# Performance work log

Measured on AMD Instinct MI355X. Metric: run time of the kernel, lower is better.

The kernel has to match this reference:

```python
import jax, jax.numpy as jnp
import numpy as np

N_HEADS = 2


def _ln(x, g, b, eps=1e-5):
    m = x.mean(-1, keepdims=True)
    v = ((x - m) ** 2).mean(-1, keepdims=True)
    return (x - m) * jax.lax.rsqrt(v + eps) * g + b


def _mha(x, in_w, in_b, out_w, out_b):
    # standard multi-head self-attention (relative/rotary branch is inert: query_pos=None)
    B, S, d = x.shape
    hd = d // N_HEADS
    qkv = x @ in_w.T + in_b
    q, k, v = jnp.split(qkv, 3, axis=-1)
    q = q.reshape(B, S, N_HEADS, hd)
    k = k.reshape(B, S, N_HEADS, hd)
    v = v.reshape(B, S, N_HEADS, hd)
    scores = jnp.einsum('bqhd,bkhd->bhqk', q, k) / jnp.sqrt(jnp.asarray(hd, x.dtype))
    attn = jax.nn.softmax(scores, axis=-1)
    o = jnp.einsum('bhqk,bkhd->bqhd', attn, v).reshape(B, S, d)
    return o @ out_w.T + out_b


def _forward(x, w1, b1, attn_in_w, attn_in_b, attn_out_w, attn_out_b, ln1_g, ln1_b,
             ffw_w1, ffw_b1, ffw_w2, ffw_b2, ln2_g, ln2_b,
             in_proj_w, conv_w, conv_b, x_proj_w, dt_proj_w, dt_proj_b, A_log, D, out_proj_w,
             w2a, b2a, w2b, b2b, w3a, b3a, w3b, b3b):
    # mlp1: (B,S,1) -> (B,S,d)
    h = x @ w1.T + b1
    # FFWRelativeSelfAttentionModule: 2 layers of post-norm MHA + FFW, take last output
    for i in range(2):
        a = _mha(h, attn_in_w[i], attn_in_b[i], attn_out_w[i], attn_out_b[i])
        h = _ln(h + a, ln1_g[i], ln1_b[i])
        f = jax.nn.relu(h @ ffw_w1[i].T + ffw_b1[i]) @ ffw_w2[i].T + ffw_b2[i]
        h = _ln(h + f, ln2_g[i], ln2_b[i])
    # Mamba block
    xz = h @ in_proj_w.T                       # (B,S,2*di)
    xm, z = jnp.split(xz, 2, axis=-1)          # (B,S,di) each
    S_len = xm.shape[1]
    dcv = conv_w.shape[1]
    xp = jnp.pad(xm, ((0, 0), (dcv - 1, 0), (0, 0)))   # causal depthwise conv1d
    xc = conv_b + sum(conv_w[:, k] * xp[:, k:k + S_len, :] for k in range(dcv))
    xc = jax.nn.silu(xc)
    xdb = xc @ x_proj_w.T                      # (B,S,dt_rank+2*N)
    dt_r = dt_proj_w.shape[1]
    N = A_log.shape[1]
    dti = xdb[..., :dt_r]
    Bm = xdb[..., dt_r:dt_r + N]
    Cm = xdb[..., dt_r + N:]
    dt = jax.nn.softplus(dti @ dt_proj_w.T + dt_proj_b)   # (B,S,di)
    A = -jnp.exp(A_log)                                    # (di,N)

    def step(hst, inp):
        dt_t, B_t, C_t, x_t = inp              # (B,di),(B,N),(B,N),(B,di)
        hst = hst * jnp.exp(dt_t[..., None] * A) + dt_t[..., None] * B_t[:, None, :] * x_t[..., None]
        y = jnp.einsum('bdn,bn->bd', hst, C_t)
        return hst, y

    h0 = jnp.zeros((xc.shape[0], A.shape[0], N), xc.dtype)
    xs = (jnp.swapaxes(dt, 0, 1), jnp.swapaxes(Bm, 0, 1),
          jnp.swapaxes(Cm, 0, 1), jnp.swapaxes(xc, 0, 1))
    _, ys = jax.lax.scan(step, h0, xs)
    y = jnp.swapaxes(ys, 0, 1) + D * xc
    y = y * jax.nn.silu(z)
    h = y @ out_proj_w.T                       # (B,S,d)
    # mlp2 (two stacked Linears, no activation) -> (B,S,1)
    o = (h @ w2a.T + b2a) @ w2b.T + b2b
    o = o.reshape(o.shape[0], -1)              # (B,9)
    # mlp3
    o = jax.nn.relu(o @ w3a.T + b3a) @ w3b.T + b3b
    return o


def setup_inputs() -> dict:
    key = jax.random.key(0)
    ks = jax.random.split(key, 16)
    d, N, dcv, di, dtr, B, S = 256, 16, 4, 512, 16, 4096, 9
    rn = lambda k, shp, s=0.02: jax.random.normal(k, shp, jnp.float32) * s
    return {
        'x': jax.random.normal(ks[0], (B, S, 1), jnp.float32),
        'w1': rn(ks[1], (d, 1), 0.5), 'b1': jnp.zeros((d,)),
        'attn_in_w': rn(ks[2], (2, 3 * d, d)), 'attn_in_b': jnp.zeros((2, 3 * d)),
        'attn_out_w': rn(ks[3], (2, d, d)), 'attn_out_b': jnp.zeros((2, d)),
        'ln1_g': jnp.ones((2, d)), 'ln1_b': jnp.zeros((2, d)),
        'ffw_w1': rn(ks[4], (2, d, d)), 'ffw_b1': jnp.zeros((2, d)),
        'ffw_w2': rn(ks[5], (2, d, d)), 'ffw_b2': jnp.zeros((2, d)),
        'ln2_g': jnp.ones((2, d)), 'ln2_b': jnp.zeros((2, d)),
        'in_proj_w': rn(ks[6], (2 * di, d)),
        'conv_w': rn(ks[7], (di, dcv), 0.2), 'conv_b': jnp.zeros((di,)),
        'x_proj_w': rn(ks[8], (dtr + 2 * N, di)),
        'dt_proj_w': rn(ks[9], (di, dtr), 0.1), 'dt_proj_b': jnp.full((di,), -4.0),
        'A_log': jnp.log(jnp.broadcast_to(jnp.arange(1, N + 1, dtype=jnp.float32), (di, N))),
        'D': jnp.ones((di,)),
        'out_proj_w': rn(ks[10], (d, di)),
        'w2a': rn(ks[11], (32, d)), 'b2a': jnp.zeros((32,)),
        'w2b': rn(ks[12], (1, 32)), 'b2b': jnp.zeros((1,)),
        'w3a': rn(ks[13], (9, 9), 0.3), 'b3a': jnp.zeros((9,)),
        'w3b': rn(ks[14], (1, 9), 0.3), 'b3b': jnp.zeros((1,)),
    }


def reference(x, w1, b1, attn_in_w, attn_in_b, attn_out_w, attn_out_b, ln1_g, ln1_b,
              ffw_w1, ffw_b1, ffw_w2, ffw_b2, ln2_g, ln2_b,
              in_proj_w, conv_w, conv_b, x_proj_w, dt_proj_w, dt_proj_b, A_log, D, out_proj_w,
              w2a, b2a, w2b, b2b, w3a, b3a, w3b, b3b):
    return _forward(x, w1, b1, attn_in_w, attn_in_b, attn_out_w, attn_out_b, ln1_g, ln1_b,
                    ffw_w1, ffw_b1, ffw_w2, ffw_b2, ln2_g, ln2_b,
                    in_proj_w, conv_w, conv_b, x_proj_w, dt_proj_w, dt_proj_b, A_log, D, out_proj_w,
                    w2a, b2a, w2b, b2b, w3a, b3a, w3b, b3b)
```

## Files before the change

kernel.cpp:

```cpp
#include <hip/hip_runtime.h>
#include <hip/hip_bf16.h>
#include <math.h>


#define BATCH 4096

typedef __attribute__((ext_vector_type(8))) short short8;
typedef __attribute__((ext_vector_type(4))) float f32x4;
typedef __attribute__((ext_vector_type(4))) unsigned short u16x4;
typedef unsigned short ushort;

__device__ __forceinline__ ushort f2bf(float f) {
    unsigned u = __float_as_uint(f);
    u += 0x7fffu + ((u >> 16) & 1u);
    return (ushort)(u >> 16);
}

__global__ __launch_bounds__(256) void convw_kernel(
    const float* __restrict__ s0, const float* __restrict__ s1,
    const float* __restrict__ s2, const float* __restrict__ s3,
    const float* __restrict__ s4, const float* __restrict__ s5,
    ushort* __restrict__ dst)
{
    int i = blockIdx.x * 256 + threadIdx.x;
    float v;
    if      (i < 393216)  v = s0[i];
    else if (i < 524288)  v = s1[i - 393216];
    else if (i < 655360)  v = s2[i - 524288];
    else if (i < 786432)  v = s3[i - 655360];
    else if (i < 1048576) v = s4[i - 786432];
    else                  v = s5[i - 1048576];
    dst[i] = f2bf(v);
}

__global__ __launch_bounds__(256) void embed_kernel(
    const float* __restrict__ x, const float* __restrict__ w1,
    const float* __restrict__ b1, float* __restrict__ h,
    ushort* __restrict__ hbf, int r0, int nr)
{
    int i = blockIdx.x * 256 + threadIdx.x;
    if (i >= nr * 256) return;
    int c  = i & 255;
    int row = i >> 8;
    float v = x[r0 + row] * w1[c] + b1[c];
    h[i] = v;
    hbf[i] = f2bf(v);
}

__global__ __launch_bounds__(256) void mgemm_kernel(
    const ushort* __restrict__ A, const ushort* __restrict__ W,
    const float* __restrict__ bias, float* __restrict__ Cf,
    ushort* __restrict__ Cb, const float* __restrict__ yin,
    int M, int N, int K, int lda, int act, int outmode)
{
    __shared__ ushort As[128 * 64];
    __shared__ ushort Bs[128 * 64];

    const int tid  = threadIdx.x;
    const int m0   = blockIdx.x * 128;
    const int n0   = blockIdx.y * 128;
    const int wid  = tid >> 6, lane = tid & 63;
    const int wr   = wid >> 1, wc = wid & 1;
    const int lrow = lane & 15, lk8 = lane >> 4, l7 = lane & 7;
    const int trow = tid >> 3, tchk = tid & 7;

    f32x4 acc[4][4];
    #pragma unroll
    for (int i = 0; i < 4; ++i)
        #pragma unroll
        for (int j = 0; j < 4; ++j)
            acc[i][j] = f32x4{0.f, 0.f, 0.f, 0.f};

    for (int k0 = 0; k0 < K; k0 += 64) {
        #pragma unroll
        for (int p = 0; p < 4; ++p) {
            const int r = p * 32 + trow;
            const short8 av = *reinterpret_cast<const short8*>(
                &A[(size_t)(m0 + r) * lda + k0 + tchk * 8]);
            const short8 wv = *reinterpret_cast<const short8*>(
                &W[(size_t)(n0 + r) * K + k0 + tchk * 8]);
            const int off = r * 64 + ((tchk ^ (r & 7)) << 3);
            *reinterpret_cast<short8*>(&As[off]) = av;
            *reinterpret_cast<short8*>(&Bs[off]) = wv;
        }
        __syncthreads();

        #pragma unroll
        for (int kh = 0; kh < 2; ++kh) {
            short8 af[4], bf[4];
            #pragma unroll
            for (int i = 0; i < 4; ++i) {
                const int ra = wr * 64 + i * 16 + lrow;
                const int rb = wc * 64 + i * 16 + lrow;
                const int sl = ((kh << 2) | lk8) ^ l7;
                af[i] = *reinterpret_cast<const short8*>(&As[ra * 64 + sl * 8]);
                bf[i] = *reinterpret_cast<const short8*>(&Bs[rb * 64 + sl * 8]);
            }
            #pragma unroll
            for (int i = 0; i < 4; ++i)
                #pragma unroll
                for (int j = 0; j < 4; ++j)
                    acc[i][j] = __builtin_amdgcn_mfma_f32_16x16x32_bf16(
                        af[i], bf[j], acc[i][j], 0, 0, 0);
        }
        __syncthreads();
    }

    const int cb = n0 + wc * 64 + lrow;
    const int rb = m0 + wr * 64 + lk8 * 4;
    float bj[4];
    #pragma unroll
    for (int j = 0; j < 4; ++j) bj[j] = bias ? bias[cb + j * 16] : 0.f;

    #pragma unroll
    for (int i = 0; i < 4; ++i) {
        #pragma unroll
        for (int r = 0; r < 4; ++r) {
            const size_t mrow = (size_t)(rb + i * 16 + r) * N;
            #pragma unroll
            for (int j = 0; j < 4; ++j) {
                float v = acc[i][j][r] + bj[j];
                const size_t idx = mrow + cb + j * 16;
                if (act == 1) v = fmaxf(v, 0.f);
                if (outmode == 0) {
                    Cf[idx] = v;
                } else if (outmode == 1) {
                    Cb[idx] = f2bf(v);
                } else {
                    const float sig = 1.f / (1.f + __expf(-v));
                    Cb[idx] = f2bf(yin[idx] * (v * sig));
                }
            }
        }
    }
}

__global__ __launch_bounds__(256) void sgemm_kernel(
    const float* __restrict__ A, const float* __restrict__ W,
    const float* __restrict__ bias, float* __restrict__ C,
    int M, int N, int K, int lda, int act)
{
    __shared__ float As[16][68];
    __shared__ float Ws[16][68];
    const int tid = threadIdx.x;
    const int m0 = blockIdx.y * 64;
    const int n0 = blockIdx.x * 64;
    const int tm = tid >> 4;
    const int tn = tid & 15;
    const int lrow = tid >> 2;
    const int lk   = (tid & 3) * 4;

    float acc[4][4] = {};

    for (int k0 = 0; k0 < K; k0 += 16) {
        {
            int m = m0 + lrow;
            float4 v = make_float4(0.f, 0.f, 0.f, 0.f);
            if (m < M) v = *reinterpret_cast<const float4*>(&A[(size_t)m * lda + k0 + lk]);
            As[lk + 0][lrow] = v.x; As[lk + 1][lrow] = v.y;
            As[lk + 2][lrow] = v.z; As[lk + 3][lrow] = v.w;
            int n = n0 + lrow;
            float4 w = make_float4(0.f, 0.f, 0.f, 0.f);
            if (n < N) w = *reinterpret_cast<const float4*>(&W[(size_t)n * K + k0 + lk]);
            Ws[lk + 0][lrow] = w.x; Ws[lk + 1][lrow] = w.y;
            Ws[lk + 2][lrow] = w.z; Ws[lk + 3][lrow] = w.w;
        }
        __syncthreads();
        #pragma unroll
        for (int k = 0; k < 16; ++k) {
            float4 av = *reinterpret_cast<const float4*>(&As[k][tm * 4]);
            float4 wv = *reinterpret_cast<const float4*>(&Ws[k][tn * 4]);
            float a[4] = {av.x, av.y, av.z, av.w};
            float w[4] = {wv.x, wv.y, wv.z, wv.w};
            #pragma unroll
            for (int i = 0; i < 4; ++i)
                #pragma unroll
                for (int j = 0; j < 4; ++j)
                    acc[i][j] = fmaf(a[i], w[j], acc[i][j]);
        }
        __syncthreads();
    }

    #pragma unroll
    for (int i = 0; i < 4; ++i) {
        int m = m0 + tm * 4 + i;
        if (m >= M) continue;
        #pragma unroll
        for (int j = 0; j < 4; ++j) {
            int n = n0 + tn * 4 + j;
            if (n >= N) continue;
            float v = acc[i][j];
            if (bias) v += bias[n];
            if (act == 1) v = fmaxf(v, 0.f);
            C[(size_t)m * N + n] = v;
        }
    }
}

__global__ __launch_bounds__(128) void attn_kernel(
    const float* __restrict__ qkv, ushort* __restrict__ o, int nb)
{
    __shared__ float q[9][132], kk[9][132], v[9][132];
    __shared__ float sc[9][12];
    const int blk = blockIdx.x;
    if (blk >= nb * 2) return;
    const int b = blk >> 1, head = blk & 1;
    const int t = threadIdx.x;
    const size_t base = (size_t)b * 9 * 768 + (size_t)head * 128;
    #pragma unroll
    for (int s = 0; s < 9; ++s) {
        q[s][t]  = qkv[base + s * 768 + t];
        kk[s][t] = qkv[base + s * 768 + 256 + t];
        v[s][t]  = qkv[base + s * 768 + 512 + t];
    }
    __syncthreads();
    if (t < 81) {
        int qi = t / 9, ki = t % 9;
        float acc = 0.f;
        #pragma unroll 8
        for (int c = 0; c < 128; ++c) acc = fmaf(q[qi][c], kk[ki][c], acc);
        sc[qi][ki] = acc * 0.08838834764831845f;
    }
    __syncthreads();
    if (t < 9) {
        float mx = -1e30f;
        #pragma unroll
        for (int k2 = 0; k2 < 9; ++k2) mx = fmaxf(mx, sc[t][k2]);
        float e[9], sum = 0.f;
        #pragma unroll
        for (int k2 = 0; k2 < 9; ++k2) { e[k2] = __expf(sc[t][k2] - mx); sum += e[k2]; }
        float inv = 1.f / sum;
        #pragma unroll
        for (int k2 = 0; k2 < 9; ++k2) sc[t][k2] = e[k2] * inv;
    }
    __syncthreads();
    #pragma unroll
    for (int qi = 0; qi < 9; ++qi) {
        float acc = 0.f;
        #pragma unroll
        for (int k2 = 0; k2 < 9; ++k2) acc = fmaf(sc[qi][k2], v[k2][t], acc);
        o[(size_t)(b * 9 + qi) * 256 + head * 128 + t] = f2bf(acc);
    }
}

__global__ __launch_bounds__(256) void ln_add_kernel(
    const float* __restrict__ h, const float* __restrict__ a,
    const float* __restrict__ g, const float* __restrict__ bb,
    float* __restrict__ out, ushort* __restrict__ outbf, int nrows)
{
    const int wave = threadIdx.x >> 6;
    const int lane = threadIdx.x & 63;
    const int row = blockIdx.x * 4 + wave;
    if (row >= nrows) return;
    const float4 hv = reinterpret_cast<const float4*>(h + (size_t)row * 256)[lane];
    const float4 av = reinterpret_cast<const float4*>(a + (size_t)row * 256)[lane];
    float x0 = hv.x + av.x, x1 = hv.y + av.y, x2 = hv.z + av.z, x3 = hv.w + av.w;
    float s  = x0 + x1 + x2 + x3;
    float sq = x0 * x0 + x1 * x1 + x2 * x2 + x3 * x3;
    #pragma unroll
    for (int off = 32; off; off >>= 1) {
        s  += __shfl_down(s, off);
        sq += __shfl_down(sq, off);
    }
    s = __shfl(s, 0); sq = __shfl(sq, 0);
    const float mean = s * (1.f / 256.f);
    const float var  = sq * (1.f / 256.f) - mean * mean;
    const float inv  = rsqrtf(var + 1e-5f);
    const float4 gv = reinterpret_cast<const float4*>(g)[lane];
    const float4 bv = reinterpret_cast<const float4*>(bb)[lane];
    float4 ov;
    ov.x = (x0 - mean) * inv * gv.x + bv.x;
    ov.y = (x1 - mean) * inv * gv.y + bv.y;
    ov.z = (x2 - mean) * inv * gv.z + bv.z;
    ov.w = (x3 - mean) * inv * gv.w + bv.w;
    reinterpret_cast<float4*>(out + (size_t)row * 256)[lane] = ov;
    u16x4 bf;
    bf.x = f2bf(ov.x); bf.y = f2bf(ov.y); bf.z = f2bf(ov.z); bf.w = f2bf(ov.w);
    reinterpret_cast<u16x4*>(outbf + (size_t)row * 256)[lane] = bf;
}

__global__ __launch_bounds__(256) void conv_silu_kernel(
    const float* __restrict__ xm, const float* __restrict__ cw,
    const float* __restrict__ cb, float* __restrict__ xc, int nr)
{
    int i = blockIdx.x * 256 + threadIdx.x;
    if (i >= nr * 512) return;
    int c = i & 511;
    int bs = i >> 9;
    int s = bs % 9, b = bs / 9;
    float acc = cb[c];
    #pragma unroll
    for (int k = 0; k < 4; ++k) {
        int sp = s + k - 3;
        if (sp >= 0) acc = fmaf(cw[c * 4 + k], xm[(size_t)(b * 9 + sp) * 512 + c], acc);
    }
    float sig = 1.f / (1.f + __expf(-acc));
    xc[(size_t)bs * 512 + c] = acc * sig;
}

__global__ __launch_bounds__(512) void scan_kernel(
    float* __restrict__ xcy, const float* __restrict__ xdb,
    const float* __restrict__ dt_w, const float* __restrict__ dt_b,
    const float* __restrict__ A_log, const float* __restrict__ Dp)
{
    __shared__ float sx[9 * 48];
    const int c = threadIdx.x;
    const int b = blockIdx.x;
    if (c < 108) {
        reinterpret_cast<float4*>(sx)[c] =
            reinterpret_cast<const float4*>(xdb + (size_t)b * 432)[c];
    }

    float wdt[16], Ar[16];
    #pragma unroll
    for (int n = 0; n < 16; n += 4) {
        float4 wv = *reinterpret_cast<const float4*>(&dt_w[c * 16 + n]);
        wdt[n] = wv.x; wdt[n + 1] = wv.y; wdt[n + 2] = wv.z; wdt[n + 3] = wv.w;
        float4 av = *reinterpret_cast<const float4*>(&A_log[c * 16 + n]);
        Ar[n] = -__expf(av.x); Ar[n + 1] = -__expf(av.y);
        Ar[n + 2] = -__expf(av.z); Ar[n + 3] = -__expf(av.w);
    }
    const float dtb = dt_b[c];
    const float Dc  = Dp[c];
    const float a1  = Ar[0];
    bool chain = true;
    #pragma unroll
    for (int n = 1; n < 16; ++n)
        chain = chain && (fabsf(Ar[n] - (float)(n + 1) * a1) <=
                          1e-3f * (float)(n + 1) * fabsf(a1));
    __syncthreads();

    float hst[16] = {};
    for (int s = 0; s < 9; ++s) {
        const float* xb = sx + s * 48;
        float dti = dtb;
        #pragma unroll
        for (int n = 0; n < 16; ++n) dti = fmaf(xb[n], wdt[n], dti);
        const float dt = (dti > 20.f) ? dti : __logf(1.f + __expf(dti));
        const size_t idx = (size_t)(b * 9 + s) * 512 + c;
        const float xv = xcy[idx];
        const float dtx = dt * xv;
        float acc = 0.f;
        if (chain) {
            const float e1 = __expf(dt * a1);
            float en = 1.f;
            #pragma unroll
            for (int n = 0; n < 16; ++n) {
                en *= e1;
                hst[n] = fmaf(hst[n], en, dtx * xb[16 + n]);
                acc = fmaf(hst[n], xb[32 + n], acc);
            }
        } else {
            #pragma unroll
            for (int n = 0; n < 16; ++n) {
                hst[n] = fmaf(hst[n], __expf(dt * Ar[n]), dtx * xb[16 + n]);
                acc = fmaf(hst[n], xb[32 + n], acc);
            }
        }
        xcy[idx] = acc + Dc * xv;
    }
}

__global__ __launch_bounds__(256) void head_kernel(
    const float* __restrict__ t32, const float* __restrict__ w2b,
    const float* __restrict__ b2b, const float* __restrict__ w3a,
    const float* __restrict__ b3a, const float* __restrict__ w3b,
    const float* __restrict__ b3b, float* __restrict__ out, int b0, int nb)
{
    int b = blockIdx.x * 256 + threadIdx.x;
    if (b >= nb) return;
    float o9[9];
    #pragma unroll
    for (int s = 0; s < 9; ++s) {
        const float* r = t32 + (size_t)(b * 9 + s) * 32;
        float acc = b2b[0];
        #pragma unroll
        for (int k = 0; k < 32; ++k) acc = fmaf(r[k], w2b[k], acc);
        o9[s] = acc;
    }
    float accout = b3b[0];
    #pragma unroll
    for (int j = 0; j < 9; ++j) {
        float rj = b3a[j];
        #pragma unroll
        for (int s = 0; s < 9; ++s) rj = fmaf(o9[s], w3a[j * 9 + s], rj);
        rj = fmaxf(rj, 0.f);
        accout = fmaf(rj, w3b[j], accout);
    }
    out[b0 + b] = accout;
}

extern "C" void kernel_launch(void* const* d_in, const int* in_sizes, int n_in,
                              void* d_out, int out_size, void* d_ws, size_t ws_size,
                              hipStream_t stream)
{
    const float* x          = (const float*)d_in[0];
    const float* w1         = (const float*)d_in[1];
    const float* b1         = (const float*)d_in[2];
    const float* attn_in_w  = (const float*)d_in[3];
    const float* attn_in_b  = (const float*)d_in[4];
    const float* attn_out_w = (const float*)d_in[5];
    const float* attn_out_b = (const float*)d_in[6];
    const float* ln1_g      = (const float*)d_in[7];
    const float* ln1_b      = (const float*)d_in[8];
    const float* ffw_w1     = (const float*)d_in[9];
    const float* ffw_b1     = (const float*)d_in[10];
    const float* ffw_w2     = (const float*)d_in[11];
    const float* ffw_b2     = (const float*)d_in[12];
    const float* ln2_g      = (const float*)d_in[13];
    const float* ln2_b      = (const float*)d_in[14];
    const float* in_proj_w  = (const float*)d_in[15];
    const float* conv_w     = (const float*)d_in[16];
    const float* conv_b     = (const float*)d_in[17];
    const float* x_proj_w   = (const float*)d_in[18];
    const float* dt_proj_w  = (const float*)d_in[19];
    const float* dt_proj_b  = (const float*)d_in[20];
    const float* A_log      = (const float*)d_in[21];
    const float* Dp         = (const float*)d_in[22];
    const float* out_proj_w = (const float*)d_in[23];
    const float* w2a        = (const float*)d_in[24];
    const float* b2a        = (const float*)d_in[25];
    const float* w2b        = (const float*)d_in[26];
    const float* b2b        = (const float*)d_in[27];
    const float* w3a        = (const float*)d_in[28];
    const float* b3a        = (const float*)d_in[29];
    const float* w3b        = (const float*)d_in[30];
    const float* b3b        = (const float*)d_in[31];
    float* out = (float*)d_out;

    const size_t WB_FLOATS = 589824;
    const size_t PER_ROW = 1792;
    int nchunks = 1;
    while (nchunks < 32 &&
           (WB_FLOATS + (size_t)(BATCH / nchunks) * 9 * PER_ROW) * sizeof(float) > ws_size)
        nchunks <<= 1;
    const int nb = BATCH / nchunks;
    const int nr = nb * 9;
    const size_t CAPR = (size_t)nr;

    ushort* WB = (ushort*)d_ws;
    float*  AR = (float*)d_ws + WB_FLOATS;

    ushort* wb_attn_in  = WB;
    ushort* wb_attn_out = WB + 393216;
    ushort* wb_ffw1     = WB + 524288;
    ushort* wb_ffw2     = WB + 655360;
    ushort* wb_inproj_x = WB + 786432;
    ushort* wb_inproj_z = WB + 917504;
    ushort* wb_outproj  = WB + 1048576;

    hipLaunchKernelGGL(convw_kernel, dim3(1179648 / 256), dim3(256), 0, stream,
                       attn_in_w, attn_out_w, ffw_w1, ffw_w2, in_proj_w,
                       out_proj_w, WB);

    auto gemm = [&](const float* A, const float* W, const float* bias, float* C,
                    int M, int N, int K, int lda, int act) {
        dim3 grid((N + 63) / 64, (M + 63) / 64);
        hipLaunchKernelGGL(sgemm_kernel, grid, dim3(256), 0, stream,
                           A, W, bias, C, M, N, K, lda, act);
    };
    auto mgemm = [&](const ushort* A, const ushort* W, const float* bias,
                     float* Cf, ushort* Cb, const float* yin,
                     int M, int N, int K, int lda, int act, int outmode) {
        dim3 grid(M / 128, N / 128);
        hipLaunchKernelGGL(mgemm_kernel, grid, dim3(256), 0, stream,
                           A, W, bias, Cf, Cb, yin, M, N, K, lda, act, outmode);
    };

    for (int ck = 0; ck < nchunks; ++ck) {
        const int b0 = ck * nb;
        const int r0 = b0 * 9;

        float*  h    = AR;
        ushort* hbf  = (ushort*)(AR + CAPR * 256);
        float*  aux  = AR + CAPR * 384;
        ushort* aobf = (ushort*)aux;
        float*  big  = AR + CAPR * 512;
        float*  qkv  = big;
        float*  aa   = big;
        ushort* f1bf = (ushort*)(big + CAPR * 256);
        float*  f2   = big + CAPR * 384;
        float*  xm   = big;
        ushort* ybf  = (ushort*)(big + CAPR * 512);
        float*  xc   = AR + CAPR * 1280;
        float*  xdb  = aux;
        float*  h2   = h;
        float*  t32  = aux;

        hipLaunchKernelGGL(embed_kernel, dim3((nr * 256 + 255) / 256), dim3(256),
                           0, stream, x, w1, b1, h, hbf, r0, nr);

        for (int i = 0; i < 2; ++i) {
            mgemm(hbf, wb_attn_in + (size_t)i * 196608, attn_in_b + i * 768,
                  qkv, nullptr, nullptr, nr, 768, 256, 256, 0, 0);
            hipLaunchKernelGGL(attn_kernel, dim3(nb * 2), dim3(128), 0, stream,
                               qkv, aobf, nb);
            mgemm(aobf, wb_attn_out + (size_t)i * 65536, attn_out_b + i * 256,
                  aa, nullptr, nullptr, nr, 256, 256, 256, 0, 0);
            hipLaunchKernelGGL(ln_add_kernel, dim3((nr + 3) / 4), dim3(256), 0, stream,
                               h, aa, ln1_g + i * 256, ln1_b + i * 256, h, hbf, nr);
            mgemm(hbf, wb_ffw1 + (size_t)i * 65536, ffw_b1 + i * 256,
                  nullptr, f1bf, nullptr, nr, 256, 256, 256, 1, 1);
            mgemm(f1bf, wb_ffw2 + (size_t)i * 65536, ffw_b2 + i * 256,
                  f2, nullptr, nullptr, nr, 256, 256, 256, 0, 0);
            hipLaunchKernelGGL(ln_add_kernel, dim3((nr + 3) / 4), dim3(256), 0, stream,
                               h, f2, ln2_g + i * 256, ln2_b + i * 256, h, hbf, nr);
        }

        mgemm(hbf, wb_inproj_x, nullptr, xm, nullptr, nullptr,
              nr, 512, 256, 256, 0, 0);
        hipLaunchKernelGGL(conv_silu_kernel, dim3((nr * 512 + 255) / 256), dim3(256),
                           0, stream, xm, conv_w, conv_b, xc, nr);
        gemm(xc, x_proj_w, nullptr, xdb, nr, 48, 512, 512, 0);
        hipLaunchKernelGGL(scan_kernel, dim3(nb), dim3(512), 0, stream,
                           xc, xdb, dt_proj_w, dt_proj_b, A_log, Dp);
        mgemm(hbf, wb_inproj_z, nullptr, nullptr, ybf, xc,
              nr, 512, 256, 256, 0, 2);
        mgemm(ybf, wb_outproj, nullptr, h2, nullptr, nullptr,
              nr, 256, 512, 512, 0, 0);
        gemm(h2, w2a, b2a, t32, nr, 32, 256, 256, 0);
        hipLaunchKernelGGL(head_kernel, dim3((nb + 255) / 256), dim3(256), 0, stream,
                           t32, w2b, b2b, w3a, b3a, w3b, b3b, out, b0, nb);
    }
}
```

Before: 791.2 us.

## Fuse conv, x_proj GEMM and scan into one Mamba kernel; store QKV as bf16

Merges the causal conv+SiLU, the fp32 x_proj GEMM and the selective scan into a single per-batch kernel. It keeps conv outputs in registers and LDS and computes x_proj with bf16 MFMA against a preconverted weight copy. It also has the QKV projection write bf16 instead of fp32, which halves the traffic into attention. This removes two launches and several global round-trips, but adds bf16 rounding to xc and QKV. Each block also reloads 48x512 weights into LDS and uses shared atomics for the split-K reduction.

```diff
diff --git a/kernel.cpp b/kernel.cpp
--- a/kernel.cpp
+++ b/kernel.cpp
@@ -15,12 +15,15 @@
     u += 0x7fffu + ((u >> 16) & 1u);
     return (ushort)(u >> 16);
 }
+__device__ __forceinline__ float bf2f(ushort u) {
+    return __uint_as_float(((unsigned)u) << 16);
+}
 
 __global__ __launch_bounds__(256) void convw_kernel(
     const float* __restrict__ s0, const float* __restrict__ s1,
     const float* __restrict__ s2, const float* __restrict__ s3,
     const float* __restrict__ s4, const float* __restrict__ s5,
-    ushort* __restrict__ dst)
+    const float* __restrict__ s6, ushort* __restrict__ dst)
 {
     int i = blockIdx.x * 256 + threadIdx.x;
     float v;
@@ -29,7 +32,8 @@
     else if (i < 655360)  v = s2[i - 524288];
     else if (i < 786432)  v = s3[i - 655360];
     else if (i < 1048576) v = s4[i - 786432];
-    else                  v = s5[i - 1048576];
+    else if (i < 1179648) v = s5[i - 1048576];
+    else                  v = s6[i - 1179648];
     dst[i] = f2bf(v);
 }
 
@@ -198,7 +202,7 @@
 }
 
 __global__ __launch_bounds__(128) void attn_kernel(
-    const float* __restrict__ qkv, ushort* __restrict__ o, int nb)
+    const ushort* __restrict__ qkv, ushort* __restrict__ o, int nb)
 {
     __shared__ float q[9][132], kk[9][132], v[9][132];
     __shared__ float sc[9][12];
@@ -209,9 +213,9 @@
     const size_t base = (size_t)b * 9 * 768 + (size_t)head * 128;
     #pragma unroll
     for (int s = 0; s < 9; ++s) {
-        q[s][t]  = qkv[base + s * 768 + t];
-        kk[s][t] = qkv[base + s * 768 + 256 + t];
-        v[s][t]  = qkv[base + s * 768 + 512 + t];
+        q[s][t]  = bf2f(qkv[base + s * 768 + t]);
+        kk[s][t] = bf2f(qkv[base + s * 768 + 256 + t]);
+        v[s][t]  = bf2f(qkv[base + s * 768 + 512 + t]);
     }
     __syncthreads();
     if (t < 81) {
@@ -279,46 +283,86 @@
     reinterpret_cast<u16x4*>(outbf + (size_t)row * 256)[lane] = bf;
 }
 
-__global__ __launch_bounds__(256) void conv_silu_kernel(
-    const float* __restrict__ xm, const float* __restrict__ cw,
-    const float* __restrict__ cb, float* __restrict__ xc, int nr)
-{
-    int i = blockIdx.x * 256 + threadIdx.x;
-    if (i >= nr * 512) return;
-    int c = i & 511;
-    int bs = i >> 9;
-    int s = bs % 9, b = bs / 9;
-    float acc = cb[c];
-    #pragma unroll
-    for (int k = 0; k < 4; ++k) {
-        int sp = s + k - 3;
-        if (sp >= 0) acc = fmaf(cw[c * 4 + k], xm[(size_t)(b * 9 + sp) * 512 + c], acc);
-    }
-    float sig = 1.f / (1.f + __expf(-acc));
-    xc[(size_t)bs * 512 + c] = acc * sig;
-}
-
-__global__ __launch_bounds__(512) void scan_kernel(
-    float* __restrict__ xcy, const float* __restrict__ xdb,
+__global__ __launch_bounds__(512) void mamba_kernel(
+    const float* __restrict__ xm, const ushort* __restrict__ wpb,
+    const float* __restrict__ cw, const float* __restrict__ cb,
     const float* __restrict__ dt_w, const float* __restrict__ dt_b,
-    const float* __restrict__ A_log, const float* __restrict__ Dp)
-{
-    __shared__ float sx[9 * 48];
-    const int c = threadIdx.x;
+    const float* __restrict__ A_log, const float* __restrict__ Dp,
+    float* __restrict__ y)
+{
+    __shared__ ushort xcbf[16 * 520];
+    __shared__ ushort wls[48 * 520];
+    __shared__ float  xdbs[16][48];
+
+    const int t = threadIdx.x, c = t;
     const int b = blockIdx.x;
-    if (c < 108) {
-        reinterpret_cast<float4*>(sx)[c] =
-            reinterpret_cast<const float4*>(xdb + (size_t)b * 432)[c];
-    }
+    const int lane = t & 63, wv = t >> 6;
+
+    #pragma unroll
+    for (int p = 0; p < 6; ++p) {
+        const int i8 = p * 512 + t;
+        const int j = i8 >> 6, k8 = i8 & 63;
+        *reinterpret_cast<short8*>(&wls[j * 520 + k8 * 8]) =
+            reinterpret_cast<const short8*>(wpb)[i8];
+    }
+
+    float xmv[9];
+    #pragma unroll
+    for (int s = 0; s < 9; ++s)
+        xmv[s] = xm[(size_t)(b * 9 + s) * 512 + c];
+    const float4 cwv4 = *reinterpret_cast<const float4*>(&cw[c * 4]);
+    const float cwv[4] = {cwv4.x, cwv4.y, cwv4.z, cwv4.w};
+    const float cbv = cb[c];
+    float xcr[9];
+    #pragma unroll
+    for (int s = 0; s < 9; ++s) {
+        float acc = cbv;
+        #pragma unroll
+        for (int k = 0; k < 4; ++k) {
+            const int sp = s + k - 3;
+            if (sp >= 0) acc = fmaf(cwv[k], xmv[sp], acc);
+        }
+        const float sig = 1.f / (1.f + __expf(-acc));
+        xcr[s] = acc * sig;
+        xcbf[s * 520 + c] = f2bf(xcr[s]);
+    }
+    if (t < 384) {
+        reinterpret_cast<float*>(xdbs)[t] = 0.f;
+        reinterpret_cast<float*>(xdbs)[t + 384] = 0.f;
+    }
+    __syncthreads();
+
+    f32x4 pacc[3];
+    #pragma unroll
+    for (int tl = 0; tl < 3; ++tl) pacc[tl] = f32x4{0.f, 0.f, 0.f, 0.f};
+    #pragma unroll
+    for (int kk2 = 0; kk2 < 2; ++kk2) {
+        const int kk = wv * 2 + kk2;
+        const short8 af = *reinterpret_cast<const short8*>(
+            &xcbf[(lane & 15) * 520 + kk * 32 + (lane >> 4) * 8]);
+        #pragma unroll
+        for (int tl = 0; tl < 3; ++tl) {
+            const short8 bf = *reinterpret_cast<const short8*>(
+                &wls[(tl * 16 + (lane & 15)) * 520 + kk * 32 + (lane >> 4) * 8]);
+            pacc[tl] = __builtin_amdgcn_mfma_f32_16x16x32_bf16(af, bf, pacc[tl], 0, 0, 0);
+        }
+    }
+    const int prow = (lane >> 4) * 4, pcol = lane & 15;
+    #pragma unroll
+    for (int tl = 0; tl < 3; ++tl)
+        #pragma unroll
+        for (int r = 0; r < 4; ++r)
+            atomicAdd(&xdbs[prow + r][tl * 16 + pcol], pacc[tl][r]);
+    __syncthreads();
 
     float wdt[16], Ar[16];
     #pragma unroll
     for (int n = 0; n < 16; n += 4) {
-        float4 wv = *reinterpret_cast<const float4*>(&dt_w[c * 16 + n]);
-        wdt[n] = wv.x; wdt[n + 1] = wv.y; wdt[n + 2] = wv.z; wdt[n + 3] = wv.w;
-        float4 av = *reinterpret_cast<const float4*>(&A_log[c * 16 + n]);
-        Ar[n] = -__expf(av.x); Ar[n + 1] = -__expf(av.y);
-        Ar[n + 2] = -__expf(av.z); Ar[n + 3] = -__expf(av.w);
+        const float4 wv4 = *reinterpret_cast<const float4*>(&dt_w[c * 16 + n]);
+        wdt[n] = wv4.x; wdt[n + 1] = wv4.y; wdt[n + 2] = wv4.z; wdt[n + 3] = wv4.w;
+        const float4 av4 = *reinterpret_cast<const float4*>(&A_log[c * 16 + n]);
+        Ar[n] = -__expf(av4.x); Ar[n + 1] = -__expf(av4.y);
+        Ar[n + 2] = -__expf(av4.z); Ar[n + 3] = -__expf(av4.w);
     }
     const float dtb = dt_b[c];
     const float Dc  = Dp[c];
@@ -328,17 +372,15 @@
     for (int n = 1; n < 16; ++n)
         chain = chain && (fabsf(Ar[n] - (float)(n + 1) * a1) <=
                           1e-3f * (float)(n + 1) * fabsf(a1));
-    __syncthreads();
 
     float hst[16] = {};
     for (int s = 0; s < 9; ++s) {
-        const float* xb = sx + s * 48;
+        const float* xb = xdbs[s];
         float dti = dtb;
         #pragma unroll
         for (int n = 0; n < 16; ++n) dti = fmaf(xb[n], wdt[n], dti);
         const float dt = (dti > 20.f) ? dti : __logf(1.f + __expf(dti));
-        const size_t idx = (size_t)(b * 9 + s) * 512 + c;
-        const float xv = xcy[idx];
+        const float xv = xcr[s];
         const float dtx = dt * xv;
         float acc = 0.f;
         if (chain) {
@@ -357,7 +399,7 @@
                 acc = fmaf(hst[n], xb[32 + n], acc);
             }
         }
-        xcy[idx] = acc + Dc * xv;
+        y[(size_t)(b * 9 + s) * 512 + c] = acc + Dc * xv;
     }
 }
 
@@ -428,7 +470,7 @@
     const float* b3b        = (const float*)d_in[31];
     float* out = (float*)d_out;
 
-    const size_t WB_FLOATS = 589824;
+    const size_t WB_FLOATS = 602112;
     const size_t PER_ROW = 1792;
     int nchunks = 1;
     while (nchunks < 32 &&
@@ -448,10 +490,11 @@
     ushort* wb_inproj_x = WB + 786432;
     ushort* wb_inproj_z = WB + 917504;
     ushort* wb_outproj  = WB + 1048576;
-
-    hipLaunchKernelGGL(convw_kernel, dim3(1179648 / 256), dim3(256), 0, stream,
+    ushort* wb_xproj    = WB + 1179648;
+
+    hipLaunchKernelGGL(convw_kernel, dim3(1204224 / 256), dim3(256), 0, stream,
                        attn_in_w, attn_out_w, ffw_w1, ffw_w2, in_proj_w,
-                       out_proj_w, WB);
+                       out_proj_w, x_proj_w, WB);
 
     auto gemm = [&](const float* A, const float* W, const float* bias, float* C,
                     int M, int N, int K, int lda, int act) {
@@ -476,14 +519,13 @@
         float*  aux  = AR + CAPR * 384;
         ushort* aobf = (ushort*)aux;
         float*  big  = AR + CAPR * 512;
-        float*  qkv  = big;
+        ushort* qkvb = (ushort*)big;
         float*  aa   = big;
         ushort* f1bf = (ushort*)(big + CAPR * 256);
         float*  f2   = big + CAPR * 384;
         float*  xm   = big;
         ushort* ybf  = (ushort*)(big + CAPR * 512);
-        float*  xc   = AR + CAPR * 1280;
-        float*  xdb  = aux;
+        float*  y    = AR + CAPR * 1280;
         float*  h2   = h;
         float*  t32  = aux;
 
@@ -492,9 +534,9 @@
 
         for (int i = 0; i < 2; ++i) {
             mgemm(hbf, wb_attn_in + (size_t)i * 196608, attn_in_b + i * 768,
-                  qkv, nullptr, nullptr, nr, 768, 256, 256, 0, 0);
+                  nullptr, qkvb, nullptr, nr, 768, 256, 256, 0, 1);
             hipLaunchKernelGGL(attn_kernel, dim3(nb * 2), dim3(128), 0, stream,
-                               qkv, aobf, nb);
+                               qkvb, aobf, nb);
             mgemm(aobf, wb_attn_out + (size_t)i * 65536, attn_out_b + i * 256,
                   aa, nullptr, nullptr, nr, 256, 256, 256, 0, 0);
             hipLaunchKernelGGL(ln_add_kernel, dim3((nr + 3) / 4), dim3(256), 0, stream,
@@ -509,12 +551,10 @@
 
         mgemm(hbf, wb_inproj_x, nullptr, xm, nullptr, nullptr,
               nr, 512, 256, 256, 0, 0);
-        hipLaunchKernelGGL(conv_silu_kernel, dim3((nr * 512 + 255) / 256), dim3(256),
-                           0, stream, xm, conv_w, conv_b, xc, nr);
-        gemm(xc, x_proj_w, nullptr, xdb, nr, 48, 512, 512, 0);
-        hipLaunchKernelGGL(scan_kernel, dim3(nb), dim3(512), 0, stream,
-                           xc, xdb, dt_proj_w, dt_proj_b, A_log, Dp);
-        mgemm(hbf, wb_inproj_z, nullptr, nullptr, ybf, xc,
+        hipLaunchKernelGGL(mamba_kernel, dim3(nb), dim3(512), 0, stream,
+                           xm, wb_xproj, conv_w, conv_b, dt_proj_w, dt_proj_b,
+                           A_log, Dp, y);
+        mgemm(hbf, wb_inproj_z, nullptr, nullptr, ybf, y,
               nr, 512, 256, 256, 0, 2);
         mgemm(ybf, wb_outproj, nullptr, h2, nullptr, nullptr,
               nr, 256, 512, 512, 0, 0);
```

Result: no change. 794.8 us (+0.5%).
